# Kernel optimization log

Measured on AMD Instinct MI355X. Metric: run time of the kernel, lower is better.

The kernel has to match this reference:

```python
import jax, jax.numpy as jnp
import numpy as np

B, C, H, W = 8, 512, 32, 32
S, E = 77, 768
NH = 8
HD = C // NH
HID = 4 * C
EPS2D = 1e-6
EPS_QK = 1.1920929e-07  # torch nn.RMSNorm default eps = fp32 machine eps


def rotate_half(x):
    p = x.reshape(*x.shape[:-1], -1, 2)
    p = jnp.stack([-p[..., 1], p[..., 0]], axis=-1)
    return p.reshape(x.shape)


def rope_1d(x):
    # x: [B, NH, S, HD] -- standard 1D RoPE over the sequence axis
    d = x.shape[-1]
    inv_freq = 1.0 / (10000.0 ** (jnp.arange(0, d, 2, dtype=jnp.float32) / d))
    ang = jnp.arange(x.shape[-2], dtype=jnp.float32)[:, None] * inv_freq[None, :]  # [S, HD/2]
    cos = jnp.repeat(jnp.cos(ang), 2, axis=-1)
    sin = jnp.repeat(jnp.sin(ang), 2, axis=-1)
    return x * cos + rotate_half(x) * sin


def rope_2d(x, freqs, h, w):
    # x: [B, NH, H*W, HD]; freqs: [HD/2, 2] learned (theta_y, theta_x)
    gy, gx = jnp.meshgrid(jnp.arange(h, dtype=jnp.float32), jnp.arange(w, dtype=jnp.float32), indexing='ij')
    ang = gy.reshape(-1)[:, None] * freqs[None, :, 0] + gx.reshape(-1)[:, None] * freqs[None, :, 1]  # [HW, HD/2]
    cos = jnp.repeat(jnp.cos(ang), 2, axis=-1)
    sin = jnp.repeat(jnp.sin(ang), 2, axis=-1)
    return x * cos + rotate_half(x) * sin


def rmsnorm_last(x, wgt, eps):
    return x * jax.lax.rsqrt(jnp.mean(x * x, axis=-1, keepdims=True) + eps) * wgt


def rmsnorm_2d(x, wgt):
    # x: [B,C,H,W], RMS over channel dim (dim=1)
    return x * jax.lax.rsqrt(jnp.mean(x * x, axis=1, keepdims=True) + EPS2D) * wgt[None, :, None, None]


def setup_inputs() -> dict:
    key = jax.random.key(0)
    ks = jax.random.split(key, 12)

    def n(k, shp, s=0.02):
        return jax.random.normal(k, shp, jnp.float32) * s

    return {
        'x': jax.random.normal(ks[0], (B, C, H, W), jnp.float32),
        'cond_seq': jax.random.normal(ks[1], (B, S, E), jnp.float32),
        'final_emb': jax.random.normal(ks[2], (B, E), jnp.float32),
        'mod_w': n(ks[3], (E, 6 * C)),
        'mod_b': jnp.zeros((6 * C,), jnp.float32),
        'norm1_scale': jnp.ones((C,), jnp.float32),
        'norm2_scale': jnp.ones((C,), jnp.float32),
        'qkv_s_w': n(ks[4], (3 * C, C)),
        'qkv_c_w': n(ks[5], (3 * C, E)),
        'rope_freqs': jax.random.normal(ks[6], (HD // 2, 2), jnp.float32),
        'qn_w': jnp.ones((HD,), jnp.float32),
        'kn_w': jnp.ones((HD,), jnp.float32),
        'out_w': n(ks[7], (C, C)),
        'out_b': jnp.zeros((C,), jnp.float32),
        'mlp_w1': n(ks[8], (HID, C)),
        'mlp_b1': jnp.zeros((HID,), jnp.float32),
        'mlp_w2': n(ks[9], (C, HID)),
        'mlp_b2': jnp.zeros((C,), jnp.float32),
    }


def reference(x, cond_seq, final_emb, mod_w, mod_b, norm1_scale, norm2_scale,
              qkv_s_w, qkv_c_w, rope_freqs, qn_w, kn_w, out_w, out_b,
              mlp_w1, mlp_b1, mlp_w2, mlp_b2):
    b, c, h, w = x.shape
    hw = h * w
    # adaLN modulation (Modulation: SiLU -> Linear -> 6 chunks)
    mod = jax.nn.silu(final_emb) @ mod_w + mod_b  # [B, 6C]
    sh1, sc1, g1, sh2, sc2, g2 = jnp.split(mod, 6, axis=-1)

    def modulate(z, shift, scale):
        return z * (1.0 + scale[:, :, None, None]) + shift[:, :, None, None]

    h_mod = modulate(rmsnorm_2d(x, norm1_scale), sh1, sc1)

    # --- FusedAttentionBlock: dual-stream (spatial + conditional) attention ---
    hm = h_mod.reshape(b, c, hw)
    qkv_s = jnp.einsum('bcn,oc->bon', hm, qkv_s_w)  # 1x1 conv, [B,3C,HW]
    q_s, k_s, v_s = jnp.split(qkv_s, 3, axis=1)

    def to_heads(t):  # [B,C,HW] -> [B,NH,HW,HD] (head-major channel layout)
        return t.reshape(b, NH, HD, hw).transpose(0, 1, 3, 2)

    q_s, k_s, v_s = to_heads(q_s), to_heads(k_s), to_heads(v_s)

    qkv_c = jnp.einsum('bse,oe->bso', cond_seq, qkv_c_w)
    qkv_c = qkv_c.reshape(b, -1, 3, NH, HD).transpose(2, 0, 3, 1, 4)
    q_c, k_c, v_c = qkv_c[0], qkv_c[1], qkv_c[2]  # [B,NH,S,HD]

    q = jnp.concatenate([rope_2d(q_s, rope_freqs, h, w), rope_1d(q_c)], axis=2)
    k = jnp.concatenate([rope_2d(k_s, rope_freqs, h, w), rope_1d(k_c)], axis=2)
    v = jnp.concatenate([v_s, v_c], axis=2)

    q = rmsnorm_last(q, qn_w, EPS_QK)
    k = rmsnorm_last(k, kn_w, EPS_QK)

    scale = 1.0 / (HD ** 0.5)
    logits = jnp.einsum('bhqd,bhkd->bhqk', q, k) * scale
    attn = jax.nn.softmax(logits, axis=-1)
    o = jnp.einsum('bhqk,bhkd->bhqd', attn, v)[:, :, :hw, :]  # spatial stream only
    o = o.transpose(0, 2, 1, 3).reshape(b, hw, c)
    o = jnp.einsum('bnc,oc->bno', o, out_w) + out_b
    attn_out = o.transpose(0, 2, 1).reshape(b, c, h, w)

    x = x + g1[:, :, None, None] * attn_out

    # --- MLP (1x1 convs, tanh-approx GELU) ---
    h2 = modulate(rmsnorm_2d(x, norm2_scale), sh2, sc2)
    m = jnp.einsum('bchw,oc->bohw', h2, mlp_w1) + mlp_b1[None, :, None, None]
    m = jax.nn.gelu(m, approximate=True)
    m = jnp.einsum('bchw,oc->bohw', m, mlp_w2) + mlp_b2[None, :, None, None]
    return x + g2[:, :, None, None] * m
```

## Files before the change

kernel.cpp:

```cpp
#include <hip/hip_runtime.h>

constexpr int BATCH = 8, CH = 512, HWN = 1024, SEQ = 77, EMB = 768;
constexpr int NHEAD = 8, HDIM = 64, HIDDEN = 2048, TTOT = 1101;
constexpr int VSTRIDE = 1152;

typedef short bhalf8 __attribute__((ext_vector_type(8)));
typedef float f32x4 __attribute__((ext_vector_type(4)));

__device__ __forceinline__ unsigned short f2bf(float f) {
    unsigned u = __builtin_bit_cast(unsigned, f);
    unsigned r = (u + 0x7fffu + ((u >> 16) & 1u)) >> 16;
    return (unsigned short)r;
}
__device__ __forceinline__ unsigned cvtpk(float a, float b) {
    unsigned r;
    asm("v_cvt_pk_bf16_f32 %0, %1, %2" : "=v"(r) : "v"(a), "v"(b));
    return r;
}
__device__ __forceinline__ float gelu_fast(float v) {
    float c = v * v * v;
    float z = fmaf(v, 2.3022082f, c * 0.10294324f);
    float e = exp2f(z) + 1.0f;
    float r;
    asm("v_rcp_f32 %0, %1" : "=v"(r) : "v"(e));
    return v - v * r;
}
__device__ __forceinline__ int swz(int b) { return b ^ ((b >> 3) & 0x70); }

__device__ __forceinline__ void gload16(const void* g, void* l) {
    __builtin_amdgcn_global_load_lds(
        (const __attribute__((address_space(1))) unsigned int*)g,
        (__attribute__((address_space(3))) unsigned int*)l, 16, 0, 0);
}

struct PrepArgs {
    const float* src[6];
    unsigned short* dst[6];
    int n[6];
    const float* freqs;
    float* ct;
    const float* emb;
    const float* mbias;
    float* mod;
    float* se;
};
__global__ void k_prep(PrepArgs a) {
    int y = blockIdx.y;
    int bx = blockIdx.x;
    int tid = threadIdx.x;
    if (y < 6) {
        int i = (bx * 256 + tid) * 4;
        if (i >= a.n[y]) return;
        float4 v = *(const float4*)&a.src[y][i];
        ushort4 o = {f2bf(v.x), f2bf(v.y), f2bf(v.z), f2bf(v.w)};
        *(ushort4*)&a.dst[y][i] = o;
    } else if (y == 6) {
        int i = bx * 256 + tid;
        if (i >= TTOT * 32) return;
        int t = i >> 5, j = i & 31;
        float ang;
        if (t < HWN) {
            ang = (float)(t >> 5) * a.freqs[2 * j] + (float)(t & 31) * a.freqs[2 * j + 1];
        } else {
            float inv = expf(-(float)j * (9.210340371976184f / 32.0f));
            ang = (float)(t - HWN) * inv;
        }
        a.ct[i * 2] = cosf(ang);
        a.ct[i * 2 + 1] = sinf(ang);
    } else {
        if (bx < 24) {
            int i = bx * 1024 + tid * 4;
            int j = i - (i / (6 * CH)) * (6 * CH);
            *(float4*)&a.mod[i] = *(const float4*)&a.mbias[j];
        } else if (bx >= 32 && bx < 38) {
            int i = (bx - 32) * 1024 + tid * 4;
            float4 v = *(const float4*)&a.emb[i];
            float4 o;
            o.x = v.x / (1.0f + expf(-v.x));
            o.y = v.y / (1.0f + expf(-v.y));
            o.z = v.z / (1.0f + expf(-v.z));
            o.w = v.w / (1.0f + expf(-v.w));
            *(float4*)&a.se[i] = o;
        }
    }
}

__global__ __launch_bounds__(256) void k_mod(const float* __restrict__ se,
        const float* __restrict__ w, float* __restrict__ mod) {
    int jb = blockIdx.x, b = blockIdx.y, ec = blockIdx.z;
    int j = jb * 256 + threadIdx.x;
    const float* sb = se + b * EMB + ec * 96;
    const float* wb = w + (size_t)(ec * 96) * (6 * CH) + j;
    float acc = 0.f;
    #pragma unroll 8
    for (int e = 0; e < 96; ++e) acc = fmaf(sb[e], wb[(size_t)e * (6 * CH)], acc);
    atomicAdd(&mod[b * (6 * CH) + j], acc);
}

__global__ __launch_bounds__(256) void k_rms2d_mod_t(const float* __restrict__ xin,
        const float* __restrict__ sw, const float* __restrict__ mod, int shoff, int scoff,
        unsigned short* __restrict__ outp) {
    __shared__ float part[4][64];
    __shared__ float rinv[64];
    int b = blockIdx.y;
    int n0 = blockIdx.x * 64;
    int tid = threadIdx.x;
    const float* xb = xin + (size_t)b * CH * HWN;
    {
        int n = n0 + (tid & 63);
        int cg = tid >> 6;
        float ss = 0.f;
        #pragma unroll 8
        for (int c = cg * 128; c < cg * 128 + 128; ++c) {
            float v = xb[(size_t)c * HWN + n];
            ss = fmaf(v, v, ss);
        }
        part[cg][tid & 63] = ss;
    }
    __syncthreads();
    if (tid < 64) {
        float s = part[0][tid] + part[1][tid] + part[2][tid] + part[3][tid];
        rinv[tid] = rsqrtf(s * (1.0f / CH) + 1e-6f);
    }
    __syncthreads();
    int n = n0 + (tid >> 2);
    int cq = tid & 3;
    float r = rinv[tid >> 2];
    const float* mb = mod + b * (6 * CH);
    unsigned short* orow = outp + ((size_t)(b * HWN + n)) * CH;
    for (int jc = 0; jc < 16; ++jc) {
        int c = cq * 128 + jc * 8;
        bhalf8 o;
        #pragma unroll
        for (int u = 0; u < 8; ++u) {
            int cc = c + u;
            float v = xb[(size_t)cc * HWN + n];
            float y = v * r * sw[cc] * (1.0f + mb[scoff + cc]) + mb[shoff + cc];
            o[u] = (short)f2bf(y);
        }
        *(bhalf8*)&orow[c] = o;
    }
}

template <int EPI, int BM, int BN>
__global__ __launch_bounds__(256) void k_gemm_mfma(
        const unsigned short* __restrict__ A, const unsigned short* __restrict__ Bt,
        void* __restrict__ OutV, int M, int N, int K,
        const float* __restrict__ bias, const float* __restrict__ gate,
        const float* __restrict__ res) {
    constexpr int WM = BM / 2, WN = BN / 2;
    constexpr int MI = WM / 16, NI = WN / 16;
    constexpr int CA = BM / 8, CB = BN / 8, CW = (CA + CB) / 4;
    constexpr int BUF = (BM + BN) * 128;
    __shared__ __align__(1024) char SM[2 * BUF];
    int tid = threadIdx.x;
    int w = tid >> 6, l = tid & 63, lg = l >> 4, ll = l & 15;
    int wr = w >> 1, wc = w & 1;
    int m0 = blockIdx.x * BM, n0 = blockIdx.y * BN;
    int r8 = l >> 3, c16 = (l & 7) * 16;
    f32x4 acc[MI][NI] = {};
    const char* Ac = (const char*)A;
    const char* Bc = (const char*)Bt;
    size_t rowBytes = (size_t)K * 2;
    int nt = K >> 6;

    auto stage = [&](int t, int bsel) {
        char* As = SM + bsel * BUF;
        char* Bs = As + BM * 128;
        int k0 = t * 64;
        #pragma unroll
        for (int i = 0; i < CW; ++i) {
            int c = w * CW + i;
            if (c < CA) {
                int row = c * 8 + r8;
                int off = c16 ^ ((row & 7) << 4);
                int ar = m0 + row;
                if (ar > M - 1) ar = M - 1;
                gload16(Ac + (size_t)ar * rowBytes + k0 * 2 + off, As + c * 1024);
            } else {
                int cc = c - CA;
                int row = cc * 8 + r8;
                int off = c16 ^ ((row & 7) << 4);
                gload16(Bc + (size_t)(n0 + row) * rowBytes + k0 * 2 + off, Bs + cc * 1024);
            }
        }
    };
    stage(0, 0);
    __syncthreads();
    int cur = 0;
    for (int t = 0; t < nt; ++t) {
        if (t + 1 < nt) stage(t + 1, cur ^ 1);
        char* As = SM + cur * BUF;
        char* Bs = As + BM * 128;
        #pragma unroll
        for (int ks = 0; ks < 2; ++ks) {
            bhalf8 af[MI], bf[NI];
            #pragma unroll
            for (int mi = 0; mi < MI; ++mi)
                af[mi] = *(const bhalf8*)(As + swz((wr * WM + mi * 16 + ll) * 128 + ks * 64 + lg * 16));
            #pragma unroll
            for (int ni = 0; ni < NI; ++ni)
                bf[ni] = *(const bhalf8*)(Bs + swz((wc * WN + ni * 16 + ll) * 128 + ks * 64 + lg * 16));
            __builtin_amdgcn_s_setprio(1);
            #pragma unroll
            for (int mi = 0; mi < MI; ++mi)
                #pragma unroll
                for (int ni = 0; ni < NI; ++ni)
                    acc[mi][ni] = __builtin_amdgcn_mfma_f32_16x16x32_bf16(af[mi], bf[ni], acc[mi][ni], 0, 0, 0);
            __builtin_amdgcn_s_setprio(0);
        }
        __syncthreads();
        cur ^= 1;
    }
    if (EPI == 2) {
        unsigned short* Out = (unsigned short*)OutV;
        #pragma unroll
        for (int mi = 0; mi < MI; ++mi)
            #pragma unroll
            for (int ni = 0; ni < NI; ++ni) {
                int col = n0 + wc * WN + ni * 16 + ll;
                float bv = bias[col];
                #pragma unroll
                for (int r = 0; r < 4; ++r) {
                    int mrow = m0 + wr * WM + mi * 16 + 4 * lg + r;
                    Out[(size_t)mrow * N + col] = f2bf(gelu_fast(acc[mi][ni][r] + bv));
                }
            }
    } else {
        float* Out = (float*)OutV;
        int bidx = m0 >> 10;
        int hw0 = m0 & 1023;
        const float* resb = res + (size_t)bidx * N * HWN;
        float* outb_ = Out + (size_t)bidx * N * HWN;
        #pragma unroll
        for (int ni = 0; ni < NI; ++ni) {
            int ch = n0 + wc * WN + ni * 16 + ll;
            float g = gate[bidx * (6 * CH) + ch];
            float bv = bias[ch];
            #pragma unroll
            for (int mi = 0; mi < MI; ++mi) {
                int t = hw0 + wr * WM + mi * 16 + 4 * lg;
                float4 r4 = *(const float4*)&resb[(size_t)ch * HWN + t];
                f32x4 a = acc[mi][ni];
                float4 o;
                o.x = r4.x + g * (a[0] + bv);
                o.y = r4.y + g * (a[1] + bv);
                o.z = r4.z + g * (a[2] + bv);
                o.w = r4.w + g * (a[3] + bv);
                *(float4*)&outb_[(size_t)ch * HWN + t] = o;
            }
        }
    }
}

template <int COND>
__global__ __launch_bounds__(256) void k_gemm_qkv(
        const unsigned short* __restrict__ A, const unsigned short* __restrict__ Bt,
        const float* __restrict__ ct, const float* __restrict__ qn,
        const float* __restrict__ kn, unsigned short* __restrict__ qb,
        unsigned short* __restrict__ kb, unsigned short* __restrict__ vT) {
    constexpr int M = COND ? 616 : 8192;
    constexpr int K = COND ? 768 : 512;
    constexpr int nOff = COND ? 512 : 0;
    __shared__ __align__(1024) char SMEM[24576];
    int tid = threadIdx.x;
    int w = tid >> 6, l = tid & 63, lg = l >> 4, ll = l & 15;
    int m0 = blockIdx.x * 128, n0 = nOff + blockIdx.y * 64;
    int r8 = l >> 3, c16 = (l & 7) * 16;
    f32x4 acc[2][4] = {};
    const char* Ac = (const char*)A;
    const char* Bc = (const char*)Bt;
    constexpr size_t rowBytes = (size_t)K * 2;
    for (int k0 = 0; k0 < K; k0 += 64) {
        __syncthreads();
        #pragma unroll
        for (int i = 0; i < 6; ++i) {
            int c = w * 6 + i;
            if (c < 16) {
                int row = c * 8 + r8;
                int off = c16 ^ ((row & 7) << 4);
                int ar = m0 + row;
                if (ar > M - 1) ar = M - 1;
                gload16(Ac + (size_t)ar * rowBytes + k0 * 2 + off, SMEM + c * 1024);
            } else {
                int cc = c - 16;
                int row = cc * 8 + r8;
                int off = c16 ^ ((row & 7) << 4);
                gload16(Bc + (size_t)(n0 + row) * rowBytes + k0 * 2 + off,
                        SMEM + 16384 + cc * 1024);
            }
        }
        __syncthreads();
        #pragma unroll
        for (int ks = 0; ks < 2; ++ks) {
            bhalf8 af[2], bf[4];
            #pragma unroll
            for (int mi = 0; mi < 2; ++mi)
                af[mi] = *(const bhalf8*)(SMEM + swz((w * 32 + mi * 16 + ll) * 128 + ks * 64 + lg * 16));
            #pragma unroll
            for (int ni = 0; ni < 4; ++ni)
                bf[ni] = *(const bhalf8*)(SMEM + 16384 + swz((ni * 16 + ll) * 128 + ks * 64 + lg * 16));
            __builtin_amdgcn_s_setprio(1);
            #pragma unroll
            for (int mi = 0; mi < 2; ++mi)
                #pragma unroll
                for (int ni = 0; ni < 4; ++ni)
                    acc[mi][ni] = __builtin_amdgcn_mfma_f32_16x16x32_bf16(af[mi], bf[ni], acc[mi][ni], 0, 0, 0);
            __builtin_amdgcn_s_setprio(0);
        }
    }
    int type = n0 >> 9;
    const float2* ct2 = (const float2*)ct;

    if (type >= 2) {
        int hd = (n0 - 1024) >> 6;
        #pragma unroll
        for (int ni = 0; ni < 4; ++ni) {
            int d = ni * 16 + ll;
            #pragma unroll
            for (int mi = 0; mi < 2; ++mi) {
                int rowL = m0 + w * 32 + mi * 16 + 4 * lg;
                if (COND == 0) {
                    int b = rowL >> 10, t = rowL & 1023;
                    uint2 pk = {cvtpk(acc[mi][ni][0], acc[mi][ni][1]),
                                cvtpk(acc[mi][ni][2], acc[mi][ni][3])};
                    *(uint2*)&vT[((size_t)(b * 8 + hd) * 64 + d) * VSTRIDE + t] = pk;
                } else {
                    #pragma unroll
                    for (int r = 0; r < 4; ++r) {
                        int row = rowL + r;
                        if (row < M) {
                            int b = row / 77, s = row - b * 77;
                            vT[((size_t)(b * 8 + hd) * 64 + d) * VSTRIDE + 1024 + s] =
                                f2bf(acc[mi][ni][r]);
                        }
                    }
                }
            }
        }
        return;
    }
    const float* wnt = (type == 0) ? qn : kn;
    float wscale = (type == 0) ? 0.18033688011112042f : 1.0f;
    float sgn = (ll & 1) ? 1.f : -1.f;
    #pragma unroll
    for (int mi = 0; mi < 2; ++mi) {
        int rowL = m0 + w * 32 + mi * 16 + 4 * lg;
        int tt[4];
        #pragma unroll
        for (int r = 0; r < 4; ++r) {
            if (COND == 0) tt[r] = (rowL + r) & 1023;
            else {
                int row = rowL + r;
                if (row > M - 1) row = M - 1;
                int b = row / 77;
                tt[r] = 1024 + (row - b * 77);
            }
        }
        #pragma unroll
        for (int ni = 0; ni < 4; ++ni) {
            int jjv = (ni * 16 + ll) >> 1;
            f32x4 a = acc[mi][ni], p;
            #pragma unroll
            for (int r = 0; r < 4; ++r) p[r] = __shfl_xor(a[r], 1);
            #pragma unroll
            for (int r = 0; r < 4; ++r) {
                float2 cs = ct2[tt[r] * 32 + jjv];
                a[r] = fmaf(sgn * p[r], cs.y, a[r] * cs.x);
            }
            acc[mi][ni] = a;
        }
        f32x4 ss = {};
        #pragma unroll
        for (int ni = 0; ni < 4; ++ni)
            #pragma unroll
            for (int r = 0; r < 4; ++r) ss[r] = fmaf(acc[mi][ni][r], acc[mi][ni][r], ss[r]);
        #pragma unroll
        for (int msk = 1; msk < 16; msk <<= 1)
            #pragma unroll
            for (int r = 0; r < 4; ++r) ss[r] += __shfl_xor(ss[r], msk);
        #pragma unroll
        for (int r = 0; r < 4; ++r)
            ss[r] = rsqrtf(ss[r] * (1.0f / 64.f) + 1.1920929e-07f) * wscale;
        #pragma unroll
        for (int ni = 0; ni < 4; ++ni) {
            float wv = wnt[ni * 16 + ll];
            #pragma unroll
            for (int r = 0; r < 4; ++r) acc[mi][ni][r] *= ss[r] * wv;
        }
    }
    __syncthreads();
    unsigned short* stg = (unsigned short*)SMEM;
    #pragma unroll
    for (int mi = 0; mi < 2; ++mi)
        #pragma unroll
        for (int ni = 0; ni < 4; ++ni) {
            int colL = ni * 16 + ll;
            int rowL = w * 32 + mi * 16 + 4 * lg;
            #pragma unroll
            for (int r = 0; r < 4; ++r)
                stg[(rowL + r) * 72 + colL] = f2bf(acc[mi][ni][r]);
        }
    __syncthreads();
    int rowO = tid >> 1, half = tid & 1;
    int rowG = m0 + rowO;
    if (COND == 1 && rowG >= M) return;
    int b, t;
    if (COND == 0) { b = rowG >> 10; t = rowG & 1023; }
    else { b = rowG / 77; t = 1024 + (rowG - b * 77); }
    unsigned short* dst;
    if (type == 0) dst = qb + ((size_t)(b * 8 + (n0 >> 6)) * HWN + t) * 64 + half * 32;
    else dst = kb + ((size_t)(b * 8 + ((n0 - 512) >> 6)) * TTOT + t) * 64 + half * 32;
    #pragma unroll
    for (int i = 0; i < 4; ++i)
        *(bhalf8*)&dst[i * 8] = *(const bhalf8*)&stg[rowO * 72 + half * 32 + i * 8];
}

__global__ __launch_bounds__(256) void k_attn_v8(const unsigned short* __restrict__ qb,
        const unsigned short* __restrict__ kbuf, const unsigned short* __restrict__ vT,
        unsigned short* __restrict__ ob) {
    __shared__ __align__(1024) char smc[40960];
    int f = blockIdx.x;
    int xcd = f & 7, n = f >> 3;
    int q0 = (n & 15) * 64;
    int bh = ((n >> 4) << 3) | xcd;
    int tid = threadIdx.x;
    int w = tid >> 6, l = tid & 63, lg = l >> 4, ll = l & 15;
    int r8 = l >> 3, c16 = (l & 7) * 16;
    bhalf8 qf[2];
    {
        const unsigned short* qbase = qb + ((size_t)bh * HWN + q0 + w * 16) * 64;
        #pragma unroll
        for (int ks = 0; ks < 2; ++ks)
            qf[ks] = *(const bhalf8*)&qbase[ll * 64 + ks * 32 + lg * 8];
    }
    bhalf8 onesf;
    #pragma unroll
    for (int i = 0; i < 8; ++i) onesf[i] = (short)0x3F80;
    f32x4 accO[4] = {};
    f32x4 Lacc = {};
    const char* kgl = (const char*)kbuf + (size_t)bh * TTOT * 128;
    const char* vgl = (const char*)vT + (size_t)bh * 64 * (VSTRIDE * 2);
    char* pw = smc + 32768 + w * 2048 + ll * 128;
    int pswz = (ll & 7) << 4;

    auto stage = [&](int kt, int bsel) {
        char* base = smc + bsel * 16384;
        #pragma unroll
        for (int i = 0; i < 4; ++i) {
            int c = w * 4 + i;
            if (c < 8) {
                int row = c * 8 + r8;
                int t = kt * 64 + row;
                if (t > TTOT - 1) t = TTOT - 1;
                gload16(kgl + (size_t)t * 128 + (c16 ^ ((row & 7) << 4)), base + c * 1024);
            } else {
                int row = (c - 8) * 8 + r8;
                gload16(vgl + (size_t)row * (VSTRIDE * 2) + kt * 128 + (c16 ^ ((row & 7) << 4)),
                        base + 8192 + (c - 8) * 1024);
            }
        }
    };
    stage(0, 0);
    __syncthreads();
    for (int kt = 0; kt < 18; ++kt) {
        int cur = kt & 1;
        if (kt < 17) stage(kt + 1, cur ^ 1);
        char* kl = smc + cur * 16384;
        char* vl = kl + 8192;
        f32x4 s[4] = {};
        __builtin_amdgcn_s_setprio(1);
        #pragma unroll
        for (int ks = 0; ks < 2; ++ks) {
            bhalf8 kf[4];
            #pragma unroll
            for (int k4 = 0; k4 < 4; ++k4)
                kf[k4] = *(const bhalf8*)(kl + swz((k4 * 16 + ll) * 128 + ks * 64 + lg * 16));
            #pragma unroll
            for (int k4 = 0; k4 < 4; ++k4)
                s[k4] = __builtin_amdgcn_mfma_f32_16x16x32_bf16(kf[k4], qf[ks], s[k4], 0, 0, 0);
        }
        __builtin_amdgcn_s_setprio(0);
        if (kt == 17) {
            int kb0 = kt * 64 + 4 * lg;
            #pragma unroll
            for (int k4 = 0; k4 < 4; ++k4)
                #pragma unroll
                for (int r = 0; r < 4; ++r)
                    if (kb0 + k4 * 16 + r >= TTOT) s[k4][r] = -1e30f;
        }
        #pragma unroll
        for (int k4 = 0; k4 < 4; ++k4) {
            float p0 = exp2f(s[k4][0]), p1 = exp2f(s[k4][1]);
            float p2 = exp2f(s[k4][2]), p3 = exp2f(s[k4][3]);
            uint2 pk = {cvtpk(p0, p1), cvtpk(p2, p3)};
            *(uint2*)(pw + ((k4 * 32 + lg * 8) ^ pswz)) = pk;
        }
        __builtin_amdgcn_s_setprio(1);
        #pragma unroll
        for (int ks = 0; ks < 2; ++ks) {
            bhalf8 vf[4];
            #pragma unroll
            for (int d4 = 0; d4 < 4; ++d4)
                vf[d4] = *(const bhalf8*)(vl + swz((d4 * 16 + ll) * 128 + ks * 64 + lg * 16));
            bhalf8 pf = *(const bhalf8*)(smc + 32768 + w * 2048 + swz(ll * 128 + ks * 64 + lg * 16));
            Lacc = __builtin_amdgcn_mfma_f32_16x16x32_bf16(onesf, pf, Lacc, 0, 0, 0);
            #pragma unroll
            for (int d4 = 0; d4 < 4; ++d4)
                accO[d4] = __builtin_amdgcn_mfma_f32_16x16x32_bf16(vf[d4], pf, accO[d4], 0, 0, 0);
        }
        __builtin_amdgcn_s_setprio(0);
        __syncthreads();
    }
    {
        float inv = 1.0f / Lacc[0];
        int orow = w * 16 + ll;
        char* po = smc + orow * 128;
        int oswz = (orow & 7) << 4;
        #pragma unroll
        for (int d4 = 0; d4 < 4; ++d4) {
            uint2 pk = {cvtpk(accO[d4][0] * inv, accO[d4][1] * inv),
                        cvtpk(accO[d4][2] * inv, accO[d4][3] * inv)};
            *(uint2*)(po + ((d4 * 32 + lg * 8) ^ oswz)) = pk;
        }
    }
    __syncthreads();
    int b = bh >> 3, h = bh & 7;
    int row = tid >> 2, seg = tid & 3;
    bhalf8 v0 = *(const bhalf8*)(smc + swz(row * 128 + seg * 32));
    bhalf8 v1 = *(const bhalf8*)(smc + swz(row * 128 + seg * 32 + 16));
    unsigned short* dst = ob + ((size_t)(b * HWN + q0 + row)) * CH + h * 64 + seg * 16;
    *(bhalf8*)&dst[0] = v0;
    *(bhalf8*)&dst[8] = v1;
}

extern "C" void kernel_launch(void* const* d_in, const int* in_sizes, int n_in,
                              void* d_out, int out_size, void* d_ws, size_t ws_size,
                              hipStream_t stream) {
    const float* x     = (const float*)d_in[0];
    const float* cond  = (const float*)d_in[1];
    const float* femb  = (const float*)d_in[2];
    const float* mod_w = (const float*)d_in[3];
    const float* mod_b = (const float*)d_in[4];
    const float* n1s   = (const float*)d_in[5];
    const float* n2s   = (const float*)d_in[6];
    const float* qkvsw = (const float*)d_in[7];
    const float* qkvcw = (const float*)d_in[8];
    const float* ropef = (const float*)d_in[9];
    const float* qn    = (const float*)d_in[10];
    const float* kn    = (const float*)d_in[11];
    const float* outw  = (const float*)d_in[12];
    const float* outb  = (const float*)d_in[13];
    const float* w1    = (const float*)d_in[14];
    const float* b1    = (const float*)d_in[15];
    const float* w2    = (const float*)d_in[16];
    const float* b2    = (const float*)d_in[17];
    float* out = (float*)d_out;
    char* W = (char*)d_ws;

    unsigned short* wqs_b = (unsigned short*)(W + 0);
    unsigned short* wqc_b = (unsigned short*)(W + 1572864);
    unsigned short* wo_b  = (unsigned short*)(W + 3932160);
    unsigned short* w1_b  = (unsigned short*)(W + 4456448);
    unsigned short* w2_b  = (unsigned short*)(W + 6553600);
    unsigned short* condb = (unsigned short*)(W + 8650752);
    float* mod            = (float*)(W + 9596928);
    float* ct             = (float*)(W + 9695232);
    unsigned short* hmod  = (unsigned short*)(W + 9977088);
    unsigned short* obuf  = hmod;
    unsigned short* qbuf  = (unsigned short*)(W + 18365696);
    unsigned short* kbuf  = (unsigned short*)(W + 26754304);
    unsigned short* vTb   = (unsigned short*)(W + 35772672);
    unsigned short* h2    = vTb;
    unsigned short* mbuf  = (unsigned short*)(W + 45209856);
    float* x1             = (float*)(W + 78764288);
    float* sebuf          = (float*)(W + 45209920);

    PrepArgs pa;
    pa.src[0] = qkvsw; pa.dst[0] = wqs_b; pa.n[0] = 1536 * 512;
    pa.src[1] = qkvcw; pa.dst[1] = wqc_b; pa.n[1] = 1536 * 768;
    pa.src[2] = outw;  pa.dst[2] = wo_b;  pa.n[2] = 512 * 512;
    pa.src[3] = w1;    pa.dst[3] = w1_b;  pa.n[3] = 2048 * 512;
    pa.src[4] = w2;    pa.dst[4] = w2_b;  pa.n[4] = 512 * 2048;
    pa.src[5] = cond;  pa.dst[5] = condb; pa.n[5] = 616 * 768;
    pa.freqs = ropef; pa.ct = ct;
    pa.emb = femb; pa.mbias = mod_b; pa.mod = mod; pa.se = sebuf;
    k_prep<<<dim3(1152, 8), 256, 0, stream>>>(pa);
    k_mod<<<dim3(12, 8, 8), 256, 0, stream>>>(sebuf, mod_w, mod);

    k_rms2d_mod_t<<<dim3(16, BATCH), 256, 0, stream>>>(x, n1s, mod, 0, 512, hmod);
    k_gemm_qkv<0><<<dim3(64, 24), 256, 0, stream>>>(hmod, wqs_b, ct, qn, kn,
                                                    qbuf, kbuf, vTb);
    k_gemm_qkv<1><<<dim3(5, 16), 256, 0, stream>>>(condb, wqc_b, ct, qn, kn,
                                                   qbuf, kbuf, vTb);
    k_attn_v8<<<dim3(1024), 256, 0, stream>>>(qbuf, kbuf, vTb, obuf);
    k_gemm_mfma<1, 128, 64><<<dim3(64, 8), 256, 0, stream>>>(
        obuf, wo_b, x1, 8192, 512, 512, outb, mod + 2 * 512, x);
    k_rms2d_mod_t<<<dim3(16, BATCH), 256, 0, stream>>>(x1, n2s, mod, 3 * 512, 4 * 512, h2);
    k_gemm_mfma<2, 128, 128><<<dim3(64, 16), 256, 0, stream>>>(
        h2, w1_b, mbuf, 8192, 2048, 512, b1, nullptr, nullptr);
    k_gemm_mfma<1, 128, 64><<<dim3(64, 8), 256, 0, stream>>>(
        mbuf, w2_b, out, 8192, 512, 2048, b2, mod + 5 * 512, x1);
}
```

Measured before the change: 220.4 us.

## Load attention K/V fragments directly from global memory instead of LDS staging

The attention kernel no longer stages K and V tiles into double-buffered shared memory with async global-to-LDS copies and per-tile block barriers. Each wave now reads its K and V MFMA fragments straight from global memory (through the caches), and only the per-wave P tile stays in LDS. This removes the per-iteration __syncthreads and cuts LDS use from 40 KB to 8 KB, which allows more blocks per CU. In exchange, the four waves of a block each fetch the same K/V data, and there is no explicit prefetch to hide global-load latency behind the MFMAs.

Result: slower. 306.7 us (+39.2%).

```diff
diff --git a/kernel.cpp b/kernel.cpp
--- a/kernel.cpp
+++ b/kernel.cpp
@@ -416,17 +416,16 @@
         *(bhalf8*)&dst[i * 8] = *(const bhalf8*)&stg[rowO * 72 + half * 32 + i * 8];
 }
 
-__global__ __launch_bounds__(256) void k_attn_v8(const unsigned short* __restrict__ qb,
+__global__ __launch_bounds__(256) void k_attn_v9(const unsigned short* __restrict__ qb,
         const unsigned short* __restrict__ kbuf, const unsigned short* __restrict__ vT,
         unsigned short* __restrict__ ob) {
-    __shared__ __align__(1024) char smc[40960];
+    __shared__ __align__(1024) char smc[8192];
     int f = blockIdx.x;
     int xcd = f & 7, n = f >> 3;
     int q0 = (n & 15) * 64;
     int bh = ((n >> 4) << 3) | xcd;
     int tid = threadIdx.x;
     int w = tid >> 6, l = tid & 63, lg = l >> 4, ll = l & 15;
-    int r8 = l >> 3, c16 = (l & 7) * 16;
     bhalf8 qf[2];
     {
         const unsigned short* qbase = qb + ((size_t)bh * HWN + q0 + w * 16) * 64;
@@ -440,47 +439,28 @@
     f32x4 accO[4] = {};
     f32x4 Lacc = {};
     const char* kgl = (const char*)kbuf + (size_t)bh * TTOT * 128;
-    const char* vgl = (const char*)vT + (size_t)bh * 64 * (VSTRIDE * 2);
-    char* pw = smc + 32768 + w * 2048 + ll * 128;
+    const char* vgl = (const char*)vT + (size_t)bh * 64 * (VSTRIDE * 2)
+                      + (size_t)ll * (VSTRIDE * 2) + lg * 16;
+    const char* kga = kgl + lg * 16;
+    char* pw = smc + w * 2048 + ll * 128;
     int pswz = (ll & 7) << 4;
-
-    auto stage = [&](int kt, int bsel) {
-        char* base = smc + bsel * 16384;
-        #pragma unroll
-        for (int i = 0; i < 4; ++i) {
-            int c = w * 4 + i;
-            if (c < 8) {
-                int row = c * 8 + r8;
-                int t = kt * 64 + row;
-                if (t > TTOT - 1) t = TTOT - 1;
-                gload16(kgl + (size_t)t * 128 + (c16 ^ ((row & 7) << 4)), base + c * 1024);
-            } else {
-                int row = (c - 8) * 8 + r8;
-                gload16(vgl + (size_t)row * (VSTRIDE * 2) + kt * 128 + (c16 ^ ((row & 7) << 4)),
-                        base + 8192 + (c - 8) * 1024);
-            }
-        }
-    };
-    stage(0, 0);
-    __syncthreads();
     for (int kt = 0; kt < 18; ++kt) {
-        int cur = kt & 1;
-        if (kt < 17) stage(kt + 1, cur ^ 1);
-        char* kl = smc + cur * 16384;
-        char* vl = kl + 8192;
         f32x4 s[4] = {};
-        __builtin_amdgcn_s_setprio(1);
         #pragma unroll
         for (int ks = 0; ks < 2; ++ks) {
             bhalf8 kf[4];
             #pragma unroll
-            for (int k4 = 0; k4 < 4; ++k4)
-                kf[k4] = *(const bhalf8*)(kl + swz((k4 * 16 + ll) * 128 + ks * 64 + lg * 16));
+            for (int k4 = 0; k4 < 4; ++k4) {
+                int key = kt * 64 + k4 * 16 + ll;
+                if (key > TTOT - 1) key = TTOT - 1;
+                kf[k4] = *(const bhalf8*)(kga + (size_t)key * 128 + ks * 64);
+            }
+            __builtin_amdgcn_s_setprio(1);
             #pragma unroll
             for (int k4 = 0; k4 < 4; ++k4)
                 s[k4] = __builtin_amdgcn_mfma_f32_16x16x32_bf16(kf[k4], qf[ks], s[k4], 0, 0, 0);
-        }
-        __builtin_amdgcn_s_setprio(0);
+            __builtin_amdgcn_s_setprio(0);
+        }
         if (kt == 17) {
             int kb0 = kt * 64 + 4 * lg;
             #pragma unroll
@@ -496,21 +476,21 @@
             uint2 pk = {cvtpk(p0, p1), cvtpk(p2, p3)};
             *(uint2*)(pw + ((k4 * 32 + lg * 8) ^ pswz)) = pk;
         }
-        __builtin_amdgcn_s_setprio(1);
         #pragma unroll
         for (int ks = 0; ks < 2; ++ks) {
             bhalf8 vf[4];
             #pragma unroll
             for (int d4 = 0; d4 < 4; ++d4)
-                vf[d4] = *(const bhalf8*)(vl + swz((d4 * 16 + ll) * 128 + ks * 64 + lg * 16));
-            bhalf8 pf = *(const bhalf8*)(smc + 32768 + w * 2048 + swz(ll * 128 + ks * 64 + lg * 16));
+                vf[d4] = *(const bhalf8*)(vgl + (size_t)(d4 * 16) * (VSTRIDE * 2)
+                                          + kt * 128 + ks * 64);
+            bhalf8 pf = *(const bhalf8*)(smc + w * 2048 + swz(ll * 128 + ks * 64 + lg * 16));
+            __builtin_amdgcn_s_setprio(1);
             Lacc = __builtin_amdgcn_mfma_f32_16x16x32_bf16(onesf, pf, Lacc, 0, 0, 0);
             #pragma unroll
             for (int d4 = 0; d4 < 4; ++d4)
                 accO[d4] = __builtin_amdgcn_mfma_f32_16x16x32_bf16(vf[d4], pf, accO[d4], 0, 0, 0);
-        }
-        __builtin_amdgcn_s_setprio(0);
-        __syncthreads();
+            __builtin_amdgcn_s_setprio(0);
+        }
     }
     {
         float inv = 1.0f / Lacc[0];
@@ -593,7 +573,7 @@
                                                     qbuf, kbuf, vTb);
     k_gemm_qkv<1><<<dim3(5, 16), 256, 0, stream>>>(condb, wqc_b, ct, qn, kn,
                                                    qbuf, kbuf, vTb);
-    k_attn_v8<<<dim3(1024), 256, 0, stream>>>(qbuf, kbuf, vTb, obuf);
+    k_attn_v9<<<dim3(1024), 256, 0, stream>>>(qbuf, kbuf, vTb, obuf);
     k_gemm_mfma<1, 128, 64><<<dim3(64, 8), 256, 0, stream>>>(
         obuf, wo_b, x1, 8192, 512, 512, outb, mod + 2 * 512, x);
     k_rms2d_mod_t<<<dim3(16, BATCH), 256, 0, stream>>>(x1, n2s, mod, 3 * 512, 4 * 512, h2);
```
